# Optimization experiments

Measured on AMD Instinct MI355X. Metric: run time of the kernel, lower is better.

Reference implementation:

```python
import jax, jax.numpy as jnp
import numpy as np

NUM_EMBEDDINGS = 1024
EMBEDDING_DIM = 64
COMMITMENT_COST = 0.25
N_TOKENS = 131072


def setup_inputs() -> dict:
    key = jax.random.key(0)
    k_in, k_emb = jax.random.split(key)
    inputs = jax.random.normal(k_in, (N_TOKENS, EMBEDDING_DIM), dtype=jnp.float32)
    # torch init: uniform(-1/K, 1/K)
    codebook = jax.random.uniform(
        k_emb, (NUM_EMBEDDINGS, EMBEDDING_DIM), dtype=jnp.float32,
        minval=-1.0 / NUM_EMBEDDINGS, maxval=1.0 / NUM_EMBEDDINGS)
    return {"inputs": inputs, "codebook": codebook}


def reference(inputs, codebook):
    sg = jax.lax.stop_gradient
    distances = (jnp.sum(inputs * inputs, axis=1, keepdims=True)
                 - 2.0 * jnp.matmul(inputs, codebook.T)
                 + jnp.sum(codebook * codebook, axis=1)[None, :])
    encoding_indices = jnp.argmin(distances, axis=1)          # [N]
    # direct gather (same math as one-hot @ codebook)
    quantized = jnp.take(codebook, encoding_indices, axis=0)  # [N, D]
    # original computes e_latent_loss and q_latent_loss identically
    # (both mse(inputs, quantized.detach())), so loss = (1 + beta) * mse
    mse = jnp.mean((sg(quantized) - inputs) ** 2)
    loss = mse + COMMITMENT_COST * mse
    # straight-through estimator
    quantized_st = inputs + sg(quantized - inputs)
    # perplexity from code usage histogram (== mean of one-hot encodings)
    counts = jax.ops.segment_sum(
        jnp.ones((inputs.shape[0],), dtype=jnp.float32),
        encoding_indices, num_segments=NUM_EMBEDDINGS)
    avg_probs = counts / inputs.shape[0]
    perplexity = jnp.exp(-jnp.sum(avg_probs * jnp.log(avg_probs + 1e-10)))
    return loss, quantized_st, perplexity, encoding_indices[:, None]
```

## Files before the change

### kernel.cpp

```cpp
#include <hip/hip_runtime.h>
#include <math.h>

#define NTOK 131072
#define KC   1024
#define DIMV 64
#define NWAVE 16
#define TPW  32
#define TPB  (NWAVE * TPW)
#define CMAX 128
#define EPSH 1e-3f

#define OUT_LOSS 0
#define OUT_Q    1
#define OUT_PERP (1 + NTOK * DIMV)
#define OUT_IDX  (2 + NTOK * DIMV)

#define WS_HIST 1
#define WS_TKT  1025
#define WS_NORM 1026
#define WS_PACK_BYTES 12288

typedef __attribute__((ext_vector_type(8))) short short8;
typedef __attribute__((ext_vector_type(4))) float f32x4;

__device__ __forceinline__ float sumsq64_np(const float v[DIMV]) {
#pragma clang fp contract(off)
  {
    float r[8];
#pragma unroll
    for (int j = 0; j < 8; ++j) r[j] = v[j] * v[j];
#pragma unroll
    for (int i = 8; i < 64; i += 8) {
#pragma unroll
      for (int j = 0; j < 8; ++j) r[j] += v[i + j] * v[i + j];
    }
    return ((r[0] + r[1]) + (r[2] + r[3])) + ((r[4] + r[5]) + (r[6] + r[7]));
  }
}

__device__ __forceinline__ unsigned short bf16rne(float f) {
  unsigned int u = __float_as_uint(f);
  return (unsigned short)((u + 0x7fffu + ((u >> 16) & 1u)) >> 16);
}

__global__ void __launch_bounds__(256)
vq_pack_kernel(const float* __restrict__ cb, float* __restrict__ ws) {
  const int e = blockIdx.x * 256 + threadIdx.x;
  if (e < 1026) ws[e] = 0.0f;
  const int tile = e >> 7, f = (e >> 6) & 1, l = e & 63;
  const int code = tile * 16 + (l & 15);
  const int kb = f * 32 + (l >> 4) * 8;
  const float4* src = reinterpret_cast<const float4*>(cb + code * DIMV + kb);
  float4 v0 = src[0], v1 = src[1];
  float v[8] = {v0.x, v0.y, v0.z, v0.w, v1.x, v1.y, v1.z, v1.w};
  unsigned int hw[4];
#pragma unroll
  for (int j = 0; j < 4; ++j) {
    hw[j] = (unsigned int)bf16rne(v[2 * j]) |
            ((unsigned int)bf16rne(v[2 * j + 1]) << 16);
  }
  char* pack = (char*)ws + WS_PACK_BYTES;
  *(uint4*)(pack + tile * 2048 + f * 1024 + l * 16) =
      make_uint4(hw[0], hw[1], hw[2], hw[3]);
  if (e < KC) {
    float row[DIMV];
    const float4* r4 = reinterpret_cast<const float4*>(cb + e * DIMV);
#pragma unroll
    for (int i = 0; i < 16; ++i) {
      float4 t = r4[i];
      row[4 * i + 0] = t.x; row[4 * i + 1] = t.y;
      row[4 * i + 2] = t.z; row[4 * i + 3] = t.w;
    }
    ws[WS_NORM + e] = sumsq64_np(row);
  }
}

__global__ void __launch_bounds__(1024)
vq_main_mfma(const float* __restrict__ xin, const float* __restrict__ cb,
             float* __restrict__ out, float* __restrict__ ws) {
  __shared__ __align__(16) char s_pack[131072];
  __shared__ float s_norm[KC];
  __shared__ unsigned int s_hist[KC];
  __shared__ unsigned int s_cand[NWAVE][CMAX];
  __shared__ unsigned long long s_key[NWAVE][TPW];
  __shared__ int s_cnt[NWAVE];
  __shared__ int s_last;

  const int tid = threadIdx.x;
  const int l   = tid & 63;
  const int wv  = tid >> 6;
  const int cls = l & 15;
  const int g   = l >> 4;
  const int blk = blockIdx.x;
  const int tb  = blk * TPB + wv * TPW;

  float* ws_mse = ws;
  unsigned int* ws_hist = (unsigned int*)ws + WS_HIST;
  unsigned int* ws_done = (unsigned int*)ws + WS_TKT;
  const float* ws_norm = ws + WS_NORM;
  const char* pack = (const char*)ws + WS_PACK_BYTES;

  {
    const uint4* src = (const uint4*)pack;
    uint4* dst = (uint4*)s_pack;
#pragma unroll
    for (int i = 0; i < 8; ++i) dst[tid + i * 1024] = src[tid + i * 1024];
  }
  s_norm[tid] = ws_norm[tid];
  s_hist[tid] = 0u;
  if (tid < NWAVE * TPW) s_key[tid >> 5][tid & 31] = ~0ull;
  if (tid < NWAVE) s_cnt[tid] = 0;
  __syncthreads();

  short8 af[2][2];
#pragma unroll
  for (int grp = 0; grp < 2; ++grp) {
    const float* xr = xin + (size_t)(tb + grp * 16 + cls) * DIMV + g * 8;
#pragma unroll
    for (int kc = 0; kc < 2; ++kc) {
      float4 v0 = *(const float4*)(xr + kc * 32);
      float4 v1 = *(const float4*)(xr + kc * 32 + 4);
      float vv[8] = {v0.x, v0.y, v0.z, v0.w, v1.x, v1.y, v1.z, v1.w};
#pragma unroll
      for (int j = 0; j < 8; ++j) af[grp][kc][j] = (short)bf16rne(vv[j]);
    }
  }

  float minv[2][4];
#pragma unroll
  for (int grp = 0; grp < 2; ++grp)
#pragma unroll
    for (int j = 0; j < 4; ++j) minv[grp][j] = INFINITY;

  short8 b0 = *(const short8*)(s_pack + l * 16);
  short8 b1 = *(const short8*)(s_pack + 1024 + l * 16);
  float nr = s_norm[cls];
#pragma unroll 2
  for (int t = 0; t < 64; ++t) {
    short8 c0 = b0, c1 = b1;
    float cc = -0.5f * nr;
    if (t < 63) {
      const char* bp = s_pack + (t + 1) * 2048 + l * 16;
      b0 = *(const short8*)(bp);
      b1 = *(const short8*)(bp + 1024);
      nr = s_norm[(t + 1) * 16 + cls];
    }
#pragma unroll
    for (int grp = 0; grp < 2; ++grp) {
      f32x4 acc = {cc, cc, cc, cc};
      acc = __builtin_amdgcn_mfma_f32_16x16x32_bf16(af[grp][0], c0, acc, 0, 0, 0);
      acc = __builtin_amdgcn_mfma_f32_16x16x32_bf16(af[grp][1], c1, acc, 0, 0, 0);
#pragma unroll
      for (int j = 0; j < 4; ++j)
        minv[grp][j] = fminf(minv[grp][j], -acc[j]);
    }
  }
#pragma unroll
  for (int mask = 1; mask < 16; mask <<= 1) {
#pragma unroll
    for (int grp = 0; grp < 2; ++grp)
#pragma unroll
      for (int j = 0; j < 4; ++j)
        minv[grp][j] = fminf(minv[grp][j], __shfl_xor(minv[grp][j], mask, 64));
  }
  float thr[2][4];
#pragma unroll
  for (int grp = 0; grp < 2; ++grp)
#pragma unroll
    for (int j = 0; j < 4; ++j) thr[grp][j] = minv[grp][j] + EPSH;

  b0 = *(const short8*)(s_pack + l * 16);
  b1 = *(const short8*)(s_pack + 1024 + l * 16);
  nr = s_norm[cls];
#pragma unroll 2
  for (int t = 0; t < 64; ++t) {
    short8 c0 = b0, c1 = b1;
    float cc = -0.5f * nr;
    if (t < 63) {
      const char* bp = s_pack + (t + 1) * 2048 + l * 16;
      b0 = *(const short8*)(bp);
      b1 = *(const short8*)(bp + 1024);
      nr = s_norm[(t + 1) * 16 + cls];
    }
#pragma unroll
    for (int grp = 0; grp < 2; ++grp) {
      f32x4 acc = {cc, cc, cc, cc};
      acc = __builtin_amdgcn_mfma_f32_16x16x32_bf16(af[grp][0], c0, acc, 0, 0, 0);
      acc = __builtin_amdgcn_mfma_f32_16x16x32_bf16(af[grp][1], c1, acc, 0, 0, 0);
#pragma unroll
      for (int j = 0; j < 4; ++j) {
        if (-acc[j] <= thr[grp][j]) {
          int pos = atomicAdd(&s_cnt[wv], 1);
          if (pos < CMAX)
            s_cand[wv][pos] =
                ((unsigned int)(grp * 16 + g * 4 + j) << 10) |
                (unsigned int)(t * 16 + cls);
        }
      }
    }
  }
  asm volatile("s_waitcnt lgkmcnt(0)" ::: "memory");
  const int cnt = s_cnt[wv];
  int n = cnt < CMAX ? cnt : CMAX;

  for (int base = 0; base < n; base += 64) {
    int i = base + l;
    if (i < n) {
      unsigned int pk = s_cand[wv][i];
      int m = (int)(pk >> 10), k = (int)(pk & 1023);
      const float4* xr4 = (const float4*)(xin + (size_t)(tb + m) * DIMV);
      const float4* er4 = (const float4*)(cb + (size_t)k * DIMV);
      float r[8];
      float dot = 0.0f;
#pragma unroll
      for (int s = 0; s < 8; ++s) {
        float4 a = xr4[2 * s], b = xr4[2 * s + 1];
        float4 ea = er4[2 * s], eb = er4[2 * s + 1];
        float xv[8] = {a.x, a.y, a.z, a.w, b.x, b.y, b.z, b.w};
        float ev[8] = {ea.x, ea.y, ea.z, ea.w, eb.x, eb.y, eb.z, eb.w};
        {
#pragma clang fp contract(off)
#pragma unroll
          for (int j = 0; j < 8; ++j) {
            float sq = xv[j] * xv[j];
            r[j] = (s == 0) ? sq : (r[j] + sq);
          }
        }
#pragma unroll
        for (int j = 0; j < 8; ++j) dot = __builtin_fmaf(ev[j], xv[j], dot);
      }
      float xx = ((r[0] + r[1]) + (r[2] + r[3])) + ((r[4] + r[5]) + (r[6] + r[7]));
      float d = (xx - 2.0f * dot) + s_norm[k];
      unsigned long long key =
          ((unsigned long long)__float_as_uint(d) << 10) | (unsigned long long)k;
      atomicMin(&s_key[wv][m], key);
    }
  }

  if (cnt > CMAX) {
    asm volatile("s_waitcnt lgkmcnt(0)" ::: "memory");
    if (l < TPW) {
      const int m = l;
      float xv[DIMV];
      const float4* xr4 = (const float4*)(xin + (size_t)(tb + m) * DIMV);
#pragma unroll
      for (int i = 0; i < 16; ++i) {
        float4 t4 = xr4[i];
        xv[4 * i + 0] = t4.x; xv[4 * i + 1] = t4.y;
        xv[4 * i + 2] = t4.z; xv[4 * i + 3] = t4.w;
      }
      float xx = sumsq64_np(xv);
      float bd = INFINITY; int bk = 0;
      for (int k = 0; k < KC; ++k) {
        const float* e = cb + (size_t)k * DIMV;
        float dot = 0.0f;
#pragma unroll
        for (int i = 0; i < DIMV; ++i) dot = __builtin_fmaf(e[i], xv[i], dot);
        float d = (xx - 2.0f * dot) + s_norm[k];
        if (d < bd) { bd = d; bk = k; }
      }
      s_key[wv][m] =
          ((unsigned long long)__float_as_uint(bd) << 10) | (unsigned long long)bk;
    }
  }
  asm volatile("s_waitcnt lgkmcnt(0)" ::: "memory");

  {
    const int m = l & 31, h = l >> 5;
    const int token = tb + m;
    unsigned long long key = s_key[wv][m];
    const int bk = (int)(key & 1023ull);
    if (h == 0) {
      out[OUT_IDX + token] = (float)bk;
      atomicAdd(&s_hist[bk], 1u);
    }
    const float4* q4 = (const float4*)(cb + (size_t)bk * DIMV + h * 32);
    const float4* x4 = (const float4*)(xin + (size_t)token * DIMV + h * 32);
    float* oq = out + OUT_Q + (size_t)token * DIMV + h * 32;
    float mse_part = 0.0f;
#pragma unroll
    for (int rr = 0; rr < 8; ++rr) {
      float4 qv = q4[rr], xv = x4[rr];
      float d0 = qv.x - xv.x, d1 = qv.y - xv.y;
      float d2 = qv.z - xv.z, d3 = qv.w - xv.w;
      float4 o;
      o.x = xv.x + d0; o.y = xv.y + d1; o.z = xv.z + d2; o.w = xv.w + d3;
      mse_part = __builtin_fmaf(d0, d0, mse_part);
      mse_part = __builtin_fmaf(d1, d1, mse_part);
      mse_part = __builtin_fmaf(d2, d2, mse_part);
      mse_part = __builtin_fmaf(d3, d3, mse_part);
      *(float4*)(oq + 4 * rr) = o;
    }
#pragma unroll
    for (int mask = 1; mask < 64; mask <<= 1)
      mse_part += __shfl_xor(mse_part, mask, 64);
    if (l == 0) atomicAdd(ws_mse, mse_part);
  }

  __syncthreads();
  {
    unsigned int c = s_hist[tid];
    if (c) atomicAdd(&ws_hist[tid], c);
  }

  if (tid == 0) {
    __threadfence();
    unsigned int tkt = atomicAdd(ws_done, 1u);
    s_last = (tkt == (unsigned int)(gridDim.x - 1)) ? 1 : 0;
  }
  __syncthreads();
  if (s_last) {
    __threadfence();
    unsigned int c = atomicAdd(&ws_hist[tid], 0u);
    float p = (float)c / 131072.0f;
    s_norm[tid] = p * logf(p + 1e-10f);
    __syncthreads();
#pragma unroll
    for (int s = 512; s > 0; s >>= 1) {
      if (tid < s) s_norm[tid] += s_norm[tid + s];
      __syncthreads();
    }
    if (tid == 0) {
      out[OUT_PERP] = expf(-s_norm[0]);
      float mse = atomicAdd(ws_mse, 0.0f) / 8388608.0f;
      out[OUT_LOSS] = mse + 0.25f * mse;
    }
  }
}

extern "C" void kernel_launch(void* const* d_in, const int* in_sizes, int n_in,
                              void* d_out, int out_size, void* d_ws, size_t ws_size,
                              hipStream_t stream) {
  (void)in_sizes; (void)n_in; (void)out_size; (void)ws_size;
  const float* xin = (const float*)d_in[0];
  const float* cb  = (const float*)d_in[1];
  float* out = (float*)d_out;
  float* ws  = (float*)d_ws;

  hipLaunchKernelGGL(vq_pack_kernel, dim3(32), dim3(256), 0, stream, cb, ws);
  hipLaunchKernelGGL(vq_main_mfma, dim3(NTOK / TPB), dim3(1024), 0, stream,
                     xin, cb, out, ws);
}
```

Measured before the change: 181.2 us.

## Split codebook into four quarters across blocks with last-arriver merge

Each block now searches only a 256-code quarter of the codebook for its 512 tokens, giving four times as many blocks with a quarter of the LDS footprint. Per-quarter argmin keys are written to scratch slots in the output buffer, and the last of the four blocks for a token set merges them and writes the outputs. The separate pack kernel is removed: each block packs its quarter to bf16 and computes norms itself, and workspace counters are cleared with a memset. The aim is higher occupancy and more parallelism, at the cost of redundant packing, a global key exchange and extra atomics and fences.

```diff
diff --git a/kernel.cpp b/kernel.cpp
--- a/kernel.cpp
+++ b/kernel.cpp
@@ -6,9 +6,12 @@
 #define DIMV 64
 #define NWAVE 16
 #define TPW  32
-#define TPB  (NWAVE * TPW)
-#define CMAX 128
-#define EPSH 1e-3f
+#define SETTOK 512
+#define NSET  (NTOK / SETTOK)
+#define QT    16
+#define QC    256
+#define CMAX  128
+#define EPSH  1e-3f
 
 #define OUT_LOSS 0
 #define OUT_Q    1
@@ -16,9 +19,8 @@
 #define OUT_IDX  (2 + NTOK * DIMV)
 
 #define WS_HIST 1
-#define WS_TKT  1025
-#define WS_NORM 1026
-#define WS_PACK_BYTES 12288
+#define WS_DONE 1025
+#define WS_TKT  1026
 
 typedef __attribute__((ext_vector_type(8))) short short8;
 typedef __attribute__((ext_vector_type(4))) float f32x4;
@@ -43,74 +45,62 @@
   return (unsigned short)((u + 0x7fffu + ((u >> 16) & 1u)) >> 16);
 }
 
-__global__ void __launch_bounds__(256)
-vq_pack_kernel(const float* __restrict__ cb, float* __restrict__ ws) {
-  const int e = blockIdx.x * 256 + threadIdx.x;
-  if (e < 1026) ws[e] = 0.0f;
-  const int tile = e >> 7, f = (e >> 6) & 1, l = e & 63;
-  const int code = tile * 16 + (l & 15);
-  const int kb = f * 32 + (l >> 4) * 8;
-  const float4* src = reinterpret_cast<const float4*>(cb + code * DIMV + kb);
-  float4 v0 = src[0], v1 = src[1];
-  float v[8] = {v0.x, v0.y, v0.z, v0.w, v1.x, v1.y, v1.z, v1.w};
-  unsigned int hw[4];
-#pragma unroll
-  for (int j = 0; j < 4; ++j) {
-    hw[j] = (unsigned int)bf16rne(v[2 * j]) |
-            ((unsigned int)bf16rne(v[2 * j + 1]) << 16);
-  }
-  char* pack = (char*)ws + WS_PACK_BYTES;
-  *(uint4*)(pack + tile * 2048 + f * 1024 + l * 16) =
-      make_uint4(hw[0], hw[1], hw[2], hw[3]);
-  if (e < KC) {
-    float row[DIMV];
-    const float4* r4 = reinterpret_cast<const float4*>(cb + e * DIMV);
-#pragma unroll
-    for (int i = 0; i < 16; ++i) {
-      float4 t = r4[i];
-      row[4 * i + 0] = t.x; row[4 * i + 1] = t.y;
-      row[4 * i + 2] = t.z; row[4 * i + 3] = t.w;
-    }
-    ws[WS_NORM + e] = sumsq64_np(row);
-  }
-}
-
 __global__ void __launch_bounds__(1024)
-vq_main_mfma(const float* __restrict__ xin, const float* __restrict__ cb,
-             float* __restrict__ out, float* __restrict__ ws) {
-  __shared__ __align__(16) char s_pack[131072];
-  __shared__ float s_norm[KC];
+vq_split(const float* __restrict__ xin, const float* __restrict__ cb,
+         float* __restrict__ out, float* __restrict__ ws) {
+  __shared__ __align__(16) char s_pack[QT * 2048];
+  __shared__ float s_norm[QC];
   __shared__ unsigned int s_hist[KC];
   __shared__ unsigned int s_cand[NWAVE][CMAX];
   __shared__ unsigned long long s_key[NWAVE][TPW];
   __shared__ int s_cnt[NWAVE];
-  __shared__ int s_last;
+  __shared__ int s_flag;
 
   const int tid = threadIdx.x;
   const int l   = tid & 63;
   const int wv  = tid >> 6;
   const int cls = l & 15;
   const int g   = l >> 4;
-  const int blk = blockIdx.x;
-  const int tb  = blk * TPB + wv * TPW;
+  const int set = blockIdx.x & (NSET - 1);
+  const int q   = blockIdx.x >> 8;
+  const int kq  = q * QC;
+  const int tb  = set * SETTOK + wv * TPW;
 
   float* ws_mse = ws;
   unsigned int* ws_hist = (unsigned int*)ws + WS_HIST;
-  unsigned int* ws_done = (unsigned int*)ws + WS_TKT;
-  const float* ws_norm = ws + WS_NORM;
-  const char* pack = (const char*)ws + WS_PACK_BYTES;
-
-  {
-    const uint4* src = (const uint4*)pack;
-    uint4* dst = (uint4*)s_pack;
-#pragma unroll
-    for (int i = 0; i < 8; ++i) dst[tid + i * 1024] = src[tid + i * 1024];
-  }
-  s_norm[tid] = ws_norm[tid];
+  unsigned int* ws_done = (unsigned int*)ws + WS_DONE;
+  unsigned int* ws_tkt  = (unsigned int*)ws + WS_TKT;
+
+  for (int c = tid; c < QT * 128; c += 1024) {
+    const int tile = c >> 7, f = (c >> 6) & 1, cl = c & 63;
+    const int code = kq + tile * 16 + (cl & 15);
+    const int kb = f * 32 + (cl >> 4) * 8;
+    const float4* src = (const float4*)(cb + (size_t)code * DIMV + kb);
+    float4 v0 = src[0], v1 = src[1];
+    float v[8] = {v0.x, v0.y, v0.z, v0.w, v1.x, v1.y, v1.z, v1.w};
+    unsigned int hw[4];
+#pragma unroll
+    for (int j = 0; j < 4; ++j) {
+      hw[j] = (unsigned int)bf16rne(v[2 * j]) |
+              ((unsigned int)bf16rne(v[2 * j + 1]) << 16);
+    }
+    *(uint4*)(s_pack + tile * 2048 + f * 1024 + cl * 16) =
+        make_uint4(hw[0], hw[1], hw[2], hw[3]);
+  }
+  if (tid < QC) {
+    float row[DIMV];
+    const float4* r4 = (const float4*)(cb + (size_t)(kq + tid) * DIMV);
+#pragma unroll
+    for (int i = 0; i < 16; ++i) {
+      float4 t = r4[i];
+      row[4 * i + 0] = t.x; row[4 * i + 1] = t.y;
+      row[4 * i + 2] = t.z; row[4 * i + 3] = t.w;
+    }
+    s_norm[tid] = sumsq64_np(row);
+  }
   s_hist[tid] = 0u;
-  if (tid < NWAVE * TPW) s_key[tid >> 5][tid & 31] = ~0ull;
+  if (tid < NWAVE * TPW) ((unsigned long long*)s_key)[tid] = ~0ull;
   if (tid < NWAVE) s_cnt[tid] = 0;
-  __syncthreads();
 
   short8 af[2][2];
 #pragma unroll
@@ -125,6 +115,7 @@
       for (int j = 0; j < 8; ++j) af[grp][kc][j] = (short)bf16rne(vv[j]);
     }
   }
+  __syncthreads();
 
   float minv[2][4];
 #pragma unroll
@@ -136,10 +127,10 @@
   short8 b1 = *(const short8*)(s_pack + 1024 + l * 16);
   float nr = s_norm[cls];
 #pragma unroll 2
-  for (int t = 0; t < 64; ++t) {
+  for (int t = 0; t < QT; ++t) {
     short8 c0 = b0, c1 = b1;
     float cc = -0.5f * nr;
-    if (t < 63) {
+    if (t < QT - 1) {
       const char* bp = s_pack + (t + 1) * 2048 + l * 16;
       b0 = *(const short8*)(bp);
       b1 = *(const short8*)(bp + 1024);
@@ -173,10 +164,10 @@
   b1 = *(const short8*)(s_pack + 1024 + l * 16);
   nr = s_norm[cls];
 #pragma unroll 2
-  for (int t = 0; t < 64; ++t) {
+  for (int t = 0; t < QT; ++t) {
     short8 c0 = b0, c1 = b1;
     float cc = -0.5f * nr;
-    if (t < 63) {
+    if (t < QT - 1) {
       const char* bp = s_pack + (t + 1) * 2048 + l * 16;
       b0 = *(const short8*)(bp);
       b1 = *(const short8*)(bp + 1024);
@@ -194,7 +185,7 @@
           if (pos < CMAX)
             s_cand[wv][pos] =
                 ((unsigned int)(grp * 16 + g * 4 + j) << 10) |
-                (unsigned int)(t * 16 + cls);
+                (unsigned int)(kq + t * 16 + cls);
         }
       }
     }
@@ -230,7 +221,7 @@
         for (int j = 0; j < 8; ++j) dot = __builtin_fmaf(ev[j], xv[j], dot);
       }
       float xx = ((r[0] + r[1]) + (r[2] + r[3])) + ((r[4] + r[5]) + (r[6] + r[7]));
-      float d = (xx - 2.0f * dot) + s_norm[k];
+      float d = (xx - 2.0f * dot) + s_norm[k - kq];
       unsigned long long key =
           ((unsigned long long)__float_as_uint(d) << 10) | (unsigned long long)k;
       atomicMin(&s_key[wv][m], key);
@@ -250,13 +241,13 @@
         xv[4 * i + 2] = t4.z; xv[4 * i + 3] = t4.w;
       }
       float xx = sumsq64_np(xv);
-      float bd = INFINITY; int bk = 0;
-      for (int k = 0; k < KC; ++k) {
+      float bd = INFINITY; int bk = kq;
+      for (int k = kq; k < kq + QC; ++k) {
         const float* e = cb + (size_t)k * DIMV;
         float dot = 0.0f;
 #pragma unroll
         for (int i = 0; i < DIMV; ++i) dot = __builtin_fmaf(e[i], xv[i], dot);
-        float d = (xx - 2.0f * dot) + s_norm[k];
+        float d = (xx - 2.0f * dot) + s_norm[k - kq];
         if (d < bd) { bd = d; bk = k; }
       }
       s_key[wv][m] =
@@ -264,11 +255,43 @@
     }
   }
   asm volatile("s_waitcnt lgkmcnt(0)" ::: "memory");
+  __syncthreads();
+
+  if (tid < SETTOK) {
+    unsigned long long key = ((unsigned long long*)s_key)[tid];
+    unsigned long long* slot = (unsigned long long*)
+        ((char*)out + 8 + (size_t)(set * SETTOK + tid) * 256 + q * 8);
+    atomicExch(slot, key);
+  }
+  __syncthreads();
+
+  if (tid == 0) {
+    __threadfence();
+    unsigned int t = atomicAdd(&ws_tkt[set], 1u);
+    s_flag = (t == 3u) ? 1 : 0;
+  }
+  __syncthreads();
+  if (!s_flag) return;
+
+  __threadfence();
+  if (tid < SETTOK) {
+    unsigned long long* srow = (unsigned long long*)
+        ((char*)out + 8 + (size_t)(set * SETTOK + tid) * 256);
+    unsigned long long k0 = atomicAdd(&srow[0], 0ull);
+    unsigned long long k1 = atomicAdd(&srow[1], 0ull);
+    unsigned long long k2 = atomicAdd(&srow[2], 0ull);
+    unsigned long long k3 = atomicAdd(&srow[3], 0ull);
+    unsigned long long key = k0 < k1 ? k0 : k1;
+    key = key < k2 ? key : k2;
+    key = key < k3 ? key : k3;
+    ((unsigned long long*)s_key)[tid] = key;
+  }
+  __syncthreads();
 
   {
-    const int m = l & 31, h = l >> 5;
-    const int token = tb + m;
-    unsigned long long key = s_key[wv][m];
+    const int tok = tid >> 1, h = tid & 1;
+    const int token = set * SETTOK + tok;
+    unsigned long long key = ((unsigned long long*)s_key)[tok];
     const int bk = (int)(key & 1023ull);
     if (h == 0) {
       out[OUT_IDX + token] = (float)bk;
@@ -296,32 +319,33 @@
       mse_part += __shfl_xor(mse_part, mask, 64);
     if (l == 0) atomicAdd(ws_mse, mse_part);
   }
-
   __syncthreads();
   {
     unsigned int c = s_hist[tid];
     if (c) atomicAdd(&ws_hist[tid], c);
   }
+  __syncthreads();
 
   if (tid == 0) {
     __threadfence();
     unsigned int tkt = atomicAdd(ws_done, 1u);
-    s_last = (tkt == (unsigned int)(gridDim.x - 1)) ? 1 : 0;
-  }
-  __syncthreads();
-  if (s_last) {
+    s_flag = (tkt == (unsigned int)(NSET - 1)) ? 1 : 0;
+  }
+  __syncthreads();
+  if (s_flag) {
     __threadfence();
+    float* scratch = (float*)s_cand;
     unsigned int c = atomicAdd(&ws_hist[tid], 0u);
     float p = (float)c / 131072.0f;
-    s_norm[tid] = p * logf(p + 1e-10f);
+    scratch[tid] = p * logf(p + 1e-10f);
     __syncthreads();
 #pragma unroll
     for (int s = 512; s > 0; s >>= 1) {
-      if (tid < s) s_norm[tid] += s_norm[tid + s];
+      if (tid < s) scratch[tid] += scratch[tid + s];
       __syncthreads();
     }
     if (tid == 0) {
-      out[OUT_PERP] = expf(-s_norm[0]);
+      out[OUT_PERP] = expf(-scratch[0]);
       float mse = atomicAdd(ws_mse, 0.0f) / 8388608.0f;
       out[OUT_LOSS] = mse + 0.25f * mse;
     }
@@ -337,7 +361,7 @@
   float* out = (float*)d_out;
   float* ws  = (float*)d_ws;
 
-  hipLaunchKernelGGL(vq_pack_kernel, dim3(32), dim3(256), 0, stream, cb, ws);
-  hipLaunchKernelGGL(vq_main_mfma, dim3(NTOK / TPB), dim3(1024), 0, stream,
+  hipMemsetAsync(d_ws, 0, sizeof(float) * (1 + KC + 1 + NSET), stream);
+  hipLaunchKernelGGL(vq_split, dim3(NSET * 4), dim3(1024), 0, stream,
                      xin, cb, out, ws);
 }
```

After: 361.1 us. +99.3%, slower.

## Halve tokens per wave and split codebook LDS staging into two halves

Applied to the files above, without the earlier changes.

Each wave now handles 16 tokens instead of 32, and the grid doubles accordingly. The codebook pack in shared memory is staged in two 64KB halves that are reloaded between passes, with the histogram aliased onto the candidate buffer, so shared memory per block drops enough to allow more resident blocks. The epilogue is remapped to four threads per token. In exchange, the pack is copied from global memory four times per block instead of once, extra block-wide barriers are added, and each loaded B fragment is reused by only one MFMA group instead of two.

```diff
diff --git a/kernel.cpp b/kernel.cpp
--- a/kernel.cpp
+++ b/kernel.cpp
@@ -5,8 +5,9 @@
 #define KC   1024
 #define DIMV 64
 #define NWAVE 16
-#define TPW  32
+#define TPW  16
 #define TPB  (NWAVE * TPW)
+#define HT   32
 #define CMAX 128
 #define EPSH 1e-3f
 
@@ -75,16 +76,16 @@
   }
 }
 
-__global__ void __launch_bounds__(1024)
+__global__ void __launch_bounds__(1024, 8)
 vq_main_mfma(const float* __restrict__ xin, const float* __restrict__ cb,
              float* __restrict__ out, float* __restrict__ ws) {
-  __shared__ __align__(16) char s_pack[131072];
+  __shared__ __align__(16) char s_pack[HT * 2048];
   __shared__ float s_norm[KC];
-  __shared__ unsigned int s_hist[KC];
+  __shared__ unsigned long long s_key[NWAVE][TPW];
   __shared__ unsigned int s_cand[NWAVE][CMAX];
-  __shared__ unsigned long long s_key[NWAVE][TPW];
   __shared__ int s_cnt[NWAVE];
-  __shared__ int s_last;
+  __shared__ int s_flag;
+  unsigned int* s_hist = (unsigned int*)&s_cand[0][0];
 
   const int tid = threadIdx.x;
   const int l   = tid & 63;
@@ -104,97 +105,102 @@
     const uint4* src = (const uint4*)pack;
     uint4* dst = (uint4*)s_pack;
 #pragma unroll
-    for (int i = 0; i < 8; ++i) dst[tid + i * 1024] = src[tid + i * 1024];
+    for (int i = 0; i < 4; ++i) dst[tid + i * 1024] = src[tid + i * 1024];
   }
   s_norm[tid] = ws_norm[tid];
-  s_hist[tid] = 0u;
-  if (tid < NWAVE * TPW) s_key[tid >> 5][tid & 31] = ~0ull;
+  if (tid < NWAVE * TPW) ((unsigned long long*)s_key)[tid] = ~0ull;
   if (tid < NWAVE) s_cnt[tid] = 0;
-  __syncthreads();
-
-  short8 af[2][2];
-#pragma unroll
-  for (int grp = 0; grp < 2; ++grp) {
-    const float* xr = xin + (size_t)(tb + grp * 16 + cls) * DIMV + g * 8;
+
+  short8 af[2];
+  {
+    const float* xr = xin + (size_t)(tb + cls) * DIMV + g * 8;
 #pragma unroll
     for (int kc = 0; kc < 2; ++kc) {
       float4 v0 = *(const float4*)(xr + kc * 32);
       float4 v1 = *(const float4*)(xr + kc * 32 + 4);
       float vv[8] = {v0.x, v0.y, v0.z, v0.w, v1.x, v1.y, v1.z, v1.w};
 #pragma unroll
-      for (int j = 0; j < 8; ++j) af[grp][kc][j] = (short)bf16rne(vv[j]);
-    }
-  }
-
-  float minv[2][4];
-#pragma unroll
-  for (int grp = 0; grp < 2; ++grp)
-#pragma unroll
-    for (int j = 0; j < 4; ++j) minv[grp][j] = INFINITY;
-
-  short8 b0 = *(const short8*)(s_pack + l * 16);
-  short8 b1 = *(const short8*)(s_pack + 1024 + l * 16);
-  float nr = s_norm[cls];
+      for (int j = 0; j < 8; ++j) af[kc][j] = (short)bf16rne(vv[j]);
+    }
+  }
+  __syncthreads();
+
+  float minv[4] = {INFINITY, INFINITY, INFINITY, INFINITY};
+#pragma unroll 1
+  for (int h = 0; h < 2; ++h) {
+    if (h) {
+      __syncthreads();
+      const uint4* src = (const uint4*)(pack + 65536);
+      uint4* dst = (uint4*)s_pack;
+#pragma unroll
+      for (int i = 0; i < 4; ++i) dst[tid + i * 1024] = src[tid + i * 1024];
+      __syncthreads();
+    }
+    short8 b0 = *(const short8*)(s_pack + l * 16);
+    short8 b1 = *(const short8*)(s_pack + 1024 + l * 16);
+    float nr = s_norm[h * 512 + cls];
 #pragma unroll 2
-  for (int t = 0; t < 64; ++t) {
-    short8 c0 = b0, c1 = b1;
-    float cc = -0.5f * nr;
-    if (t < 63) {
-      const char* bp = s_pack + (t + 1) * 2048 + l * 16;
-      b0 = *(const short8*)(bp);
-      b1 = *(const short8*)(bp + 1024);
-      nr = s_norm[(t + 1) * 16 + cls];
-    }
-#pragma unroll
-    for (int grp = 0; grp < 2; ++grp) {
+    for (int t = 0; t < HT; ++t) {
+      short8 c0 = b0, c1 = b1;
+      float cc = -0.5f * nr;
+      if (t < HT - 1) {
+        const char* bp = s_pack + (t + 1) * 2048 + l * 16;
+        b0 = *(const short8*)(bp);
+        b1 = *(const short8*)(bp + 1024);
+        nr = s_norm[h * 512 + (t + 1) * 16 + cls];
+      }
       f32x4 acc = {cc, cc, cc, cc};
-      acc = __builtin_amdgcn_mfma_f32_16x16x32_bf16(af[grp][0], c0, acc, 0, 0, 0);
-      acc = __builtin_amdgcn_mfma_f32_16x16x32_bf16(af[grp][1], c1, acc, 0, 0, 0);
+      acc = __builtin_amdgcn_mfma_f32_16x16x32_bf16(af[0], c0, acc, 0, 0, 0);
+      acc = __builtin_amdgcn_mfma_f32_16x16x32_bf16(af[1], c1, acc, 0, 0, 0);
 #pragma unroll
       for (int j = 0; j < 4; ++j)
-        minv[grp][j] = fminf(minv[grp][j], -acc[j]);
+        minv[j] = fminf(minv[j], -acc[j]);
     }
   }
 #pragma unroll
   for (int mask = 1; mask < 16; mask <<= 1) {
 #pragma unroll
-    for (int grp = 0; grp < 2; ++grp)
-#pragma unroll
-      for (int j = 0; j < 4; ++j)
-        minv[grp][j] = fminf(minv[grp][j], __shfl_xor(minv[grp][j], mask, 64));
-  }
-  float thr[2][4];
-#pragma unroll
-  for (int grp = 0; grp < 2; ++grp)
-#pragma unroll
-    for (int j = 0; j < 4; ++j) thr[grp][j] = minv[grp][j] + EPSH;
-
-  b0 = *(const short8*)(s_pack + l * 16);
-  b1 = *(const short8*)(s_pack + 1024 + l * 16);
-  nr = s_norm[cls];
+    for (int j = 0; j < 4; ++j)
+      minv[j] = fminf(minv[j], __shfl_xor(minv[j], mask, 64));
+  }
+  float thr[4];
+#pragma unroll
+  for (int j = 0; j < 4; ++j) thr[j] = minv[j] + EPSH;
+
+#pragma unroll 1
+  for (int h = 0; h < 2; ++h) {
+    {
+      __syncthreads();
+      const uint4* src = (const uint4*)(pack + h * 65536);
+      uint4* dst = (uint4*)s_pack;
+#pragma unroll
+      for (int i = 0; i < 4; ++i) dst[tid + i * 1024] = src[tid + i * 1024];
+      __syncthreads();
+    }
+    short8 b0 = *(const short8*)(s_pack + l * 16);
+    short8 b1 = *(const short8*)(s_pack + 1024 + l * 16);
+    float nr = s_norm[h * 512 + cls];
 #pragma unroll 2
-  for (int t = 0; t < 64; ++t) {
-    short8 c0 = b0, c1 = b1;
-    float cc = -0.5f * nr;
-    if (t < 63) {
-      const char* bp = s_pack + (t + 1) * 2048 + l * 16;
-      b0 = *(const short8*)(bp);
-      b1 = *(const short8*)(bp + 1024);
-      nr = s_norm[(t + 1) * 16 + cls];
-    }
-#pragma unroll
-    for (int grp = 0; grp < 2; ++grp) {
+    for (int t = 0; t < HT; ++t) {
+      short8 c0 = b0, c1 = b1;
+      float cc = -0.5f * nr;
+      if (t < HT - 1) {
+        const char* bp = s_pack + (t + 1) * 2048 + l * 16;
+        b0 = *(const short8*)(bp);
+        b1 = *(const short8*)(bp + 1024);
+        nr = s_norm[h * 512 + (t + 1) * 16 + cls];
+      }
       f32x4 acc = {cc, cc, cc, cc};
-      acc = __builtin_amdgcn_mfma_f32_16x16x32_bf16(af[grp][0], c0, acc, 0, 0, 0);
-      acc = __builtin_amdgcn_mfma_f32_16x16x32_bf16(af[grp][1], c1, acc, 0, 0, 0);
+      acc = __builtin_amdgcn_mfma_f32_16x16x32_bf16(af[0], c0, acc, 0, 0, 0);
+      acc = __builtin_amdgcn_mfma_f32_16x16x32_bf16(af[1], c1, acc, 0, 0, 0);
 #pragma unroll
       for (int j = 0; j < 4; ++j) {
-        if (-acc[j] <= thr[grp][j]) {
+        if (-acc[j] <= thr[j]) {
           int pos = atomicAdd(&s_cnt[wv], 1);
           if (pos < CMAX)
             s_cand[wv][pos] =
-                ((unsigned int)(grp * 16 + g * 4 + j) << 10) |
-                (unsigned int)(t * 16 + cls);
+                ((unsigned int)(g * 4 + j) << 10) |
+                (unsigned int)((h * HT + t) * 16 + cls);
         }
       }
     }
@@ -263,23 +269,25 @@
           ((unsigned long long)__float_as_uint(bd) << 10) | (unsigned long long)bk;
     }
   }
-  asm volatile("s_waitcnt lgkmcnt(0)" ::: "memory");
-
+  __syncthreads();
+
+  if (tid < KC) s_hist[tid] = 0u;
+  __syncthreads();
   {
-    const int m = l & 31, h = l >> 5;
-    const int token = tb + m;
-    unsigned long long key = s_key[wv][m];
+    const int tok = tid >> 2, sub = tid & 3;
+    const int token = blk * TPB + tok;
+    unsigned long long key = ((unsigned long long*)s_key)[tok];
     const int bk = (int)(key & 1023ull);
-    if (h == 0) {
+    if (sub == 0) {
       out[OUT_IDX + token] = (float)bk;
       atomicAdd(&s_hist[bk], 1u);
     }
-    const float4* q4 = (const float4*)(cb + (size_t)bk * DIMV + h * 32);
-    const float4* x4 = (const float4*)(xin + (size_t)token * DIMV + h * 32);
-    float* oq = out + OUT_Q + (size_t)token * DIMV + h * 32;
+    const float4* q4 = (const float4*)(cb + (size_t)bk * DIMV + sub * 16);
+    const float4* x4 = (const float4*)(xin + (size_t)token * DIMV + sub * 16);
+    float* oq = out + OUT_Q + (size_t)token * DIMV + sub * 16;
     float mse_part = 0.0f;
 #pragma unroll
-    for (int rr = 0; rr < 8; ++rr) {
+    for (int rr = 0; rr < 4; ++rr) {
       float4 qv = q4[rr], xv = x4[rr];
       float d0 = qv.x - xv.x, d1 = qv.y - xv.y;
       float d2 = qv.z - xv.z, d3 = qv.w - xv.w;
@@ -296,20 +304,20 @@
       mse_part += __shfl_xor(mse_part, mask, 64);
     if (l == 0) atomicAdd(ws_mse, mse_part);
   }
-
-  __syncthreads();
-  {
+  __syncthreads();
+  if (tid < KC) {
     unsigned int c = s_hist[tid];
     if (c) atomicAdd(&ws_hist[tid], c);
   }
+  __syncthreads();
 
   if (tid == 0) {
     __threadfence();
     unsigned int tkt = atomicAdd(ws_done, 1u);
-    s_last = (tkt == (unsigned int)(gridDim.x - 1)) ? 1 : 0;
-  }
-  __syncthreads();
-  if (s_last) {
+    s_flag = (tkt == (unsigned int)(gridDim.x - 1)) ? 1 : 0;
+  }
+  __syncthreads();
+  if (s_flag) {
     __threadfence();
     unsigned int c = atomicAdd(&ws_hist[tid], 0u);
     float p = (float)c / 131072.0f;
```

Result: slower. 250.1 us (+38.0%).

## Split argmin and epilogue into separate kernels with key handoff through output

Applied to the files above, without the earlier changes.

Splits the fused kernel in two. The MFMA argmin kernel now only writes each token's packed distance/index key into the quantized-output region as scratch. A new lightweight 256-thread epilogue kernel then does the gather, the straight-through output, the MSE and histogram atomics, and the final perplexity and loss. The aim is to take the memory-bound epilogue out of the large-LDS, 1024-thread argmin blocks so it runs at higher occupancy. In exchange it adds a kernel launch plus an extra write and read of the keys, and relies on the epilogue reading each token's key before its own quantized stores overwrite that scratch slot.

```diff
diff --git a/kernel.cpp b/kernel.cpp
--- a/kernel.cpp
+++ b/kernel.cpp
@@ -76,15 +76,13 @@
 }
 
 __global__ void __launch_bounds__(1024)
-vq_main_mfma(const float* __restrict__ xin, const float* __restrict__ cb,
-             float* __restrict__ out, float* __restrict__ ws) {
+vq_argmin(const float* __restrict__ xin, const float* __restrict__ cb,
+          float* __restrict__ out, float* __restrict__ ws) {
   __shared__ __align__(16) char s_pack[131072];
   __shared__ float s_norm[KC];
-  __shared__ unsigned int s_hist[KC];
   __shared__ unsigned int s_cand[NWAVE][CMAX];
   __shared__ unsigned long long s_key[NWAVE][TPW];
   __shared__ int s_cnt[NWAVE];
-  __shared__ int s_last;
 
   const int tid = threadIdx.x;
   const int l   = tid & 63;
@@ -94,9 +92,6 @@
   const int blk = blockIdx.x;
   const int tb  = blk * TPB + wv * TPW;
 
-  float* ws_mse = ws;
-  unsigned int* ws_hist = (unsigned int*)ws + WS_HIST;
-  unsigned int* ws_done = (unsigned int*)ws + WS_TKT;
   const float* ws_norm = ws + WS_NORM;
   const char* pack = (const char*)ws + WS_PACK_BYTES;
 
@@ -107,8 +102,7 @@
     for (int i = 0; i < 8; ++i) dst[tid + i * 1024] = src[tid + i * 1024];
   }
   s_norm[tid] = ws_norm[tid];
-  s_hist[tid] = 0u;
-  if (tid < NWAVE * TPW) s_key[tid >> 5][tid & 31] = ~0ull;
+  if (tid < NWAVE * TPW) ((unsigned long long*)s_key)[tid] = ~0ull;
   if (tid < NWAVE) s_cnt[tid] = 0;
   __syncthreads();
 
@@ -263,65 +257,92 @@
           ((unsigned long long)__float_as_uint(bd) << 10) | (unsigned long long)bk;
     }
   }
-  asm volatile("s_waitcnt lgkmcnt(0)" ::: "memory");
-
-  {
-    const int m = l & 31, h = l >> 5;
-    const int token = tb + m;
-    unsigned long long key = s_key[wv][m];
-    const int bk = (int)(key & 1023ull);
-    if (h == 0) {
-      out[OUT_IDX + token] = (float)bk;
-      atomicAdd(&s_hist[bk], 1u);
-    }
-    const float4* q4 = (const float4*)(cb + (size_t)bk * DIMV + h * 32);
-    const float4* x4 = (const float4*)(xin + (size_t)token * DIMV + h * 32);
-    float* oq = out + OUT_Q + (size_t)token * DIMV + h * 32;
-    float mse_part = 0.0f;
-#pragma unroll
-    for (int rr = 0; rr < 8; ++rr) {
-      float4 qv = q4[rr], xv = x4[rr];
-      float d0 = qv.x - xv.x, d1 = qv.y - xv.y;
-      float d2 = qv.z - xv.z, d3 = qv.w - xv.w;
-      float4 o;
-      o.x = xv.x + d0; o.y = xv.y + d1; o.z = xv.z + d2; o.w = xv.w + d3;
-      mse_part = __builtin_fmaf(d0, d0, mse_part);
-      mse_part = __builtin_fmaf(d1, d1, mse_part);
-      mse_part = __builtin_fmaf(d2, d2, mse_part);
-      mse_part = __builtin_fmaf(d3, d3, mse_part);
-      *(float4*)(oq + 4 * rr) = o;
-    }
-#pragma unroll
-    for (int mask = 1; mask < 64; mask <<= 1)
-      mse_part += __shfl_xor(mse_part, mask, 64);
-    if (l == 0) atomicAdd(ws_mse, mse_part);
-  }
-
-  __syncthreads();
-  {
-    unsigned int c = s_hist[tid];
-    if (c) atomicAdd(&ws_hist[tid], c);
-  }
+  __syncthreads();
+
+  if (tid < TPB) {
+    const int token = blk * TPB + tid;
+    *(unsigned long long*)((char*)out + 8 + (size_t)token * 256) =
+        ((unsigned long long*)s_key)[tid];
+  }
+}
+
+__global__ void __launch_bounds__(256)
+vq_epilogue(const float* __restrict__ xin, const float* __restrict__ cb,
+            float* __restrict__ out, float* __restrict__ ws) {
+  __shared__ unsigned int s_hist[KC];
+  __shared__ float s_red[256];
+  __shared__ int s_flag;
+  const int tid = threadIdx.x;
+  const int l   = tid & 63;
+
+  float* ws_mse = ws;
+  unsigned int* ws_hist = (unsigned int*)ws + WS_HIST;
+  unsigned int* ws_done = (unsigned int*)ws + WS_TKT;
+
+  for (int k = tid; k < KC; k += 256) s_hist[k] = 0u;
+  __syncthreads();
+
+  const int tok = blockIdx.x * 64 + (tid >> 2);
+  const int sub = tid & 3;
+  unsigned long long key =
+      *(const unsigned long long*)((const char*)out + 8 + (size_t)tok * 256);
+  const int bk = (int)(key & 1023ull);
+  if (sub == 0) {
+    out[OUT_IDX + tok] = (float)bk;
+    atomicAdd(&s_hist[bk], 1u);
+  }
+  const float4* q4 = (const float4*)(cb + (size_t)bk * DIMV + sub * 16);
+  const float4* x4 = (const float4*)(xin + (size_t)tok * DIMV + sub * 16);
+  float* oq = out + OUT_Q + (size_t)tok * DIMV + sub * 16;
+  float mse_part = 0.0f;
+#pragma unroll
+  for (int rr = 0; rr < 4; ++rr) {
+    float4 qv = q4[rr], xv = x4[rr];
+    float d0 = qv.x - xv.x, d1 = qv.y - xv.y;
+    float d2 = qv.z - xv.z, d3 = qv.w - xv.w;
+    float4 o;
+    o.x = xv.x + d0; o.y = xv.y + d1; o.z = xv.z + d2; o.w = xv.w + d3;
+    mse_part = __builtin_fmaf(d0, d0, mse_part);
+    mse_part = __builtin_fmaf(d1, d1, mse_part);
+    mse_part = __builtin_fmaf(d2, d2, mse_part);
+    mse_part = __builtin_fmaf(d3, d3, mse_part);
+    *(float4*)(oq + 4 * rr) = o;
+  }
+#pragma unroll
+  for (int mask = 1; mask < 64; mask <<= 1)
+    mse_part += __shfl_xor(mse_part, mask, 64);
+  if (l == 0) atomicAdd(ws_mse, mse_part);
+
+  __syncthreads();
+  for (int k = tid; k < KC; k += 256) {
+    unsigned int c = s_hist[k];
+    if (c) atomicAdd(&ws_hist[k], c);
+  }
+  __syncthreads();
 
   if (tid == 0) {
     __threadfence();
     unsigned int tkt = atomicAdd(ws_done, 1u);
-    s_last = (tkt == (unsigned int)(gridDim.x - 1)) ? 1 : 0;
-  }
-  __syncthreads();
-  if (s_last) {
+    s_flag = (tkt == (unsigned int)(gridDim.x - 1)) ? 1 : 0;
+  }
+  __syncthreads();
+  if (s_flag) {
     __threadfence();
-    unsigned int c = atomicAdd(&ws_hist[tid], 0u);
-    float p = (float)c / 131072.0f;
-    s_norm[tid] = p * logf(p + 1e-10f);
+    float term = 0.0f;
+    for (int k = tid; k < KC; k += 256) {
+      unsigned int c = atomicAdd(&ws_hist[k], 0u);
+      float p = (float)c / 131072.0f;
+      term += p * logf(p + 1e-10f);
+    }
+    s_red[tid] = term;
     __syncthreads();
 #pragma unroll
-    for (int s = 512; s > 0; s >>= 1) {
-      if (tid < s) s_norm[tid] += s_norm[tid + s];
+    for (int s = 128; s > 0; s >>= 1) {
+      if (tid < s) s_red[tid] += s_red[tid + s];
       __syncthreads();
     }
     if (tid == 0) {
-      out[OUT_PERP] = expf(-s_norm[0]);
+      out[OUT_PERP] = expf(-s_red[0]);
       float mse = atomicAdd(ws_mse, 0.0f) / 8388608.0f;
       out[OUT_LOSS] = mse + 0.25f * mse;
     }
@@ -338,6 +359,8 @@
   float* ws  = (float*)d_ws;
 
   hipLaunchKernelGGL(vq_pack_kernel, dim3(32), dim3(256), 0, stream, cb, ws);
-  hipLaunchKernelGGL(vq_main_mfma, dim3(NTOK / TPB), dim3(1024), 0, stream,
+  hipLaunchKernelGGL(vq_argmin, dim3(NTOK / TPB), dim3(1024), 0, stream,
                      xin, cb, out, ws);
-}
+  hipLaunchKernelGGL(vq_epilogue, dim3(NTOK / 64), dim3(256), 0, stream,
+                     xin, cb, out, ws);
+}
```

New measurement: 289.5 us. 1.6x slower.
